# Kernel optimization log

Measured on AMD Instinct MI355X. Metric: run time of the kernel, lower is better.

## Reference

```python
import jax, jax.numpy as jnp
import numpy as np

B, S, D, MEM, STRIDE = 8, 8192, 128, 128, 64

def setup_inputs() -> dict:
    key = jax.random.key(0)
    ks = jax.random.split(key, 6)
    scale = 0.01  # matches nn.init.normal_(w, 0.0, 0.01)
    x = jax.random.normal(ks[0], (B, S, D), dtype=jnp.float32)
    Wq = scale * jax.random.normal(ks[1], (D, D), dtype=jnp.float32)
    Wk = scale * jax.random.normal(ks[2], (D, D), dtype=jnp.float32)
    Wv = scale * jax.random.normal(ks[3], (MEM, D), dtype=jnp.float32)
    Wg_w = jnp.zeros((1, D), dtype=jnp.float32)       # W_g weight init zeros
    Wg_b = jnp.full((1,), -2.0, dtype=jnp.float32)    # W_g bias init -2.0
    Wout = scale * jax.random.normal(ks[4], (D, MEM), dtype=jnp.float32)
    return {"x": x, "Wq": Wq, "Wk": Wk, "Wv": Wv, "Wg_w": Wg_w, "Wg_b": Wg_b, "Wout": Wout}

def reference(x, Wq, Wk, Wv, Wg_w, Wg_b, Wout):
    b, s, d = x.shape
    nC = s // STRIDE  # S assumed divisible by stride
    q = x @ Wq.T                                  # [B,S,D]
    k = x @ Wk.T                                  # [B,S,D]
    v = x @ Wv.T                                  # [B,S,MEM]
    g = jax.nn.sigmoid(x @ Wg_w.T + Wg_b)         # [B,S,1]
    # chunk: leading scan axis nC
    qc = q.reshape(b, nC, STRIDE, d).transpose(1, 0, 2, 3)
    kc = k.reshape(b, nC, STRIDE, d).transpose(1, 0, 2, 3)
    vc = v.reshape(b, nC, STRIDE, MEM).transpose(1, 0, 2, 3)
    gc = g.reshape(b, nC, STRIDE, 1).transpose(1, 0, 2, 3)

    def step(M, chunk):
        qch, kch, vch, gch = chunk
        reads = jnp.einsum('bsd,bdm->bsm', qch, M)              # read before write
        write = jnp.einsum('bsd,bsm->bdm', kch * gch, vch)      # gated outer-product
        avg_gate = gch.mean(axis=1, keepdims=True)              # [B,1,1]
        M_new = (1.0 - avg_gate) * M + write
        return M_new, reads

    M0 = jnp.zeros((b, d, MEM), dtype=x.dtype)
    _, reads = jax.lax.scan(step, M0, (qc, kc, vc, gc))         # [nC,B,STRIDE,MEM]
    out = reads.transpose(1, 0, 2, 3).reshape(b, s, MEM)
    return out @ Wout.T                                         # [B,S,D]
```

## Files before the change

### kernel.cpp

```cpp
#include <hip/hip_runtime.h>

#define Bn 8
#define Sn 8192
#define Dn 128
#define NCn 128

typedef _Float16 f16;
typedef f16 f16x2 __attribute__((ext_vector_type(2)));
typedef f16 f16x4 __attribute__((ext_vector_type(4)));
typedef float f32x4 __attribute__((ext_vector_type(4)));

static __device__ __forceinline__ f32x4 mfma16(f16x4 a, f16x4 b, f32x4 c) {
  return __builtin_amdgcn_mfma_f32_16x16x16f16(a, b, c, 0, 0, 0);
}

union UU { uint4 u; f16x2 h[4]; };


__global__ __launch_bounds__(64) void k_prep(
    const float* __restrict__ Wq, const float* __restrict__ Wk,
    const float* __restrict__ Wv, const float* __restrict__ Wout,
    f16* __restrict__ Amat, f16* __restrict__ r2) {
  const int blk = blockIdx.x;
  const int which = blk >> 6;
  const int t = blk & 63, ti = t >> 3, tj = t & 7;
  const int lane = threadIdx.x & 63, r16 = lane & 15, g4 = lane >> 4;
  f32x4 acc = {};
  if (which == 0) {
#pragma unroll
    for (int kk = 0; kk < 8; ++kk) {
      f16x4 af, bf;
#pragma unroll
      for (int j = 0; j < 4; ++j) {
        af[j] = (f16)Wq[(kk * 16 + g4 * 4 + j) * 128 + ti * 16 + r16];
        bf[j] = (f16)Wk[(kk * 16 + g4 * 4 + j) * 128 + tj * 16 + r16];
      }
      acc = mfma16(af, bf, acc);
    }
  } else {
#pragma unroll
    for (int kk = 0; kk < 8; ++kk) {
      f16x4 af, bf;
      float4 a4 = *(const float4*)(Wout + (ti * 16 + r16) * 128 + kk * 16 + g4 * 4);
      af[0] = (f16)a4.x; af[1] = (f16)a4.y; af[2] = (f16)a4.z; af[3] = (f16)a4.w;
#pragma unroll
      for (int j = 0; j < 4; ++j)
        bf[j] = (f16)Wv[(kk * 16 + g4 * 4 + j) * 128 + tj * 16 + r16];
      acc = mfma16(af, bf, acc);
    }
  }
  f16* dst = which ? r2 : Amat;
#pragma unroll
  for (int j = 0; j < 4; ++j)
    dst[(ti * 16 + g4 * 4 + j) * 128 + tj * 16 + r16] = (f16)acc[j];
}

__global__ __launch_bounds__(512, 8) void k_phase1(
    const float* __restrict__ x, const float* __restrict__ gw, const float* __restrict__ gb,
    const f16* __restrict__ Amat, const f16* __restrict__ r2,
    f16x4* __restrict__ wtg, float* __restrict__ gavg) {
  __shared__ __align__(16) f16 Xs[64][136];
  __shared__ __align__(16) f16x4 vP[2048];
  __shared__ float gs[64];
  const int h = blockIdx.x;
  const int grp = h & 127, m = h >> 7;
  const int b = grp >> 4, seg = grp & 15;
  const int c = seg * 8 + m;
  const int tid = threadIdx.x;
  {
    int s = tid >> 3, sub = tid & 7;
    const float* xrow = x + ((size_t)b * Sn + (size_t)c * 64 + s) * Dn;
    float gpart = 0.f;
#pragma unroll
    for (int i = 0; i < 4; ++i) {
      int col = sub * 4 + i * 32;
      float4 v = *(const float4*)(xrow + col);
      float4 g = *(const float4*)(gw + col);
      gpart += v.x * g.x + v.y * g.y + v.z * g.z + v.w * g.w;
      f16x4 hh = {(f16)v.x, (f16)v.y, (f16)v.z, (f16)v.w};
      *(f16x4*)&Xs[s][col] = hh;
    }
    gpart += __shfl_xor(gpart, 1);
    gpart += __shfl_xor(gpart, 2);
    gpart += __shfl_xor(gpart, 4);
    if (sub == 0) gs[s] = 1.f / (1.f + __expf(-(gpart + gb[0])));
  }
  __syncthreads();
  if (tid == 0) {
    float sum = 0.f;
#pragma unroll
    for (int i = 0; i < 64; ++i) sum += gs[i];
    gavg[b * NCn + c] = sum * (1.f / 64.f);
  }
  const int w = tid >> 6, lane = tid & 63, r16 = lane & 15, g4 = lane >> 4;

  f32x4 uacc[4] = {}, vacc[4] = {};
#pragma unroll
  for (int kk = 0; kk < 8; ++kk) {
    f16x4 bu = *(const f16x4*)&Amat[(w * 16 + r16) * 128 + kk * 16 + g4 * 4];
    f16x4 bv = *(const f16x4*)&r2[(w * 16 + r16) * 128 + kk * 16 + g4 * 4];
#pragma unroll
    for (int mr = 0; mr < 4; ++mr) {
      f16x4 af = *(f16x4*)&Xs[mr * 16 + r16][kk * 16 + g4 * 4];
      uacc[mr] = mfma16(af, bu, uacc[mr]);
      vacc[mr] = mfma16(af, bv, vacc[mr]);
    }
  }
  f16x4 ua[4];
#pragma unroll
  for (int mr = 0; mr < 4; ++mr) {
    float g0 = gs[mr * 16 + g4 * 4 + 0], g1 = gs[mr * 16 + g4 * 4 + 1];
    float g2 = gs[mr * 16 + g4 * 4 + 2], g3 = gs[mr * 16 + g4 * 4 + 3];
    f16x4 uh = {(f16)(uacc[mr][0] * g0), (f16)(uacc[mr][1] * g1),
                (f16)(uacc[mr][2] * g2), (f16)(uacc[mr][3] * g3)};
    ua[mr] = uh;
    f16x4 vh = {(f16)vacc[mr][0], (f16)vacc[mr][1], (f16)vacc[mr][2], (f16)vacc[mr][3]};
    vP[(mr * 8 + w) * 64 + lane] = vh;
  }
  __syncthreads();

  f32x4 z[8] = {};
#pragma unroll
  for (int ks = 0; ks < 4; ++ks)
#pragma unroll
    for (int ct = 0; ct < 8; ++ct)
      z[ct] = mfma16(ua[ks], vP[(ks * 8 + ct) * 64 + lane], z[ct]);

  f16x4* wdst = wtg + (size_t)(b * NCn + c) * 4096;
#pragma unroll
  for (int ct = 0; ct < 8; ++ct) {
    f16x4 zh = {(f16)z[ct][0], (f16)z[ct][1], (f16)z[ct][2], (f16)z[ct][3]};
    wdst[(w * 8 + ct) * 64 + lane] = zh;
  }
}

__global__ __launch_bounds__(256) void k_scan(
    const uint* __restrict__ wtg, const float* __restrict__ gavg, uint* __restrict__ pbuf) {
  const int blk = blockIdx.x;
  const int b = blk >> 5;
  const int e = (blk & 31) * 256 + threadIdx.x;
  const uint* wp = wtg + (size_t)b * (NCn * 8192) + e;
  uint* pp = pbuf + (size_t)b * (15 * 8192) + e;
  const float* ga = gavg + b * NCn;
  float M0 = 0.f, M1 = 0.f;
  uint ubuf[32];
  float abuf[32];
#pragma unroll
  for (int i = 0; i < 32; ++i) {
    ubuf[i] = wp[(size_t)i * 8192];
    abuf[i] = ga[i];
  }
  for (int g = 0; g < 4; ++g) {
    uint un[32];
    float an[32];
    if (g < 3) {
#pragma unroll
      for (int i = 0; i < 32; ++i) {
        un[i] = wp[(size_t)((g + 1) * 32 + i) * 8192];
        an[i] = ga[(g + 1) * 32 + i];
      }
    }
#pragma unroll
    for (int i = 0; i < 32; ++i) {
      int cc = g * 32 + i;
      f16x2 wv = __builtin_bit_cast(f16x2, ubuf[i]);
      float dd = 1.f - abuf[i];
      M0 = dd * M0 + (float)wv[0];
      M1 = dd * M1 + (float)wv[1];
      if ((cc & 7) == 7 && cc < 120) {
        f16x2 mv = {(f16)M0, (f16)M1};
        pp[(size_t)(cc >> 3) * 8192] = __builtin_bit_cast(uint, mv);
      }
    }
    if (g < 3) {
#pragma unroll
      for (int i = 0; i < 32; ++i) { ubuf[i] = un[i]; abuf[i] = an[i]; }
    }
  }
}

__global__ __launch_bounds__(512, 8) void k_out(
    const float* __restrict__ x, const uint4* __restrict__ wtg4,
    const uint4* __restrict__ pbuf4, const float* __restrict__ gavg,
    float* __restrict__ outp) {
  __shared__ __align__(16) f16 Xs[64][136];
  __shared__ __align__(16) f16x4 zP[2048];
  const int h = blockIdx.x;
  const int grp = h & 127, m = h >> 7;
  const int b = grp >> 4, seg = grp & 15;
  const int c = seg * 8 + m;
  const int tid = threadIdx.x;
  {
    int s = tid >> 3, sub = tid & 7;
    const float* xrow = x + ((size_t)b * Sn + (size_t)c * 64 + s) * Dn;
#pragma unroll
    for (int i = 0; i < 4; ++i) {
      int col = sub * 4 + i * 32;
      float4 v = *(const float4*)(xrow + col);
      f16x4 hh = {(f16)v.x, (f16)v.y, (f16)v.z, (f16)v.w};
      *(f16x4*)&Xs[s][col] = hh;
    }
  }
  float d[8], sfac[8];
#pragma unroll
  for (int t = 0; t < 8; ++t)
    d[t] = (t < m) ? (1.f - gavg[b * NCn + seg * 8 + t]) : 1.f;
  sfac[7] = 1.f;
#pragma unroll
  for (int t = 6; t >= 0; --t) sfac[t] = sfac[t + 1] * d[t + 1];
  const float sP = sfac[0] * d[0];

  const uint4* Zbase = wtg4 + (size_t)(b * NCn + seg * 8) * 2048;
  const uint4* Pp = pbuf4 + (size_t)(b * 15 + (seg > 0 ? seg - 1 : 0)) * 2048;

  const int w = tid >> 6, lane = tid & 63, r16 = lane & 15, g4 = lane >> 4;
  const int mr = w & 3, cb = (w >> 2) * 4;
  f32x4 acc[4] = {};

#pragma unroll
  for (int half = 0; half < 2; ++half) {
    if (half) __syncthreads();
#pragma unroll
    for (int i = 0; i < 2; ++i) {
      int idx = tid + i * 512;
      int src = half * 1024 + idx;
      float a8[8] = {0.f, 0.f, 0.f, 0.f, 0.f, 0.f, 0.f, 0.f};
      if (seg > 0) {
        UU z; z.u = Pp[src];
#pragma unroll
        for (int q = 0; q < 4; ++q) {
          a8[2 * q] += sP * (float)z.h[q][0];
          a8[2 * q + 1] += sP * (float)z.h[q][1];
        }
      }
#pragma unroll
      for (int t = 0; t < 8; ++t)
        if (t < m) {
          UU z; z.u = Zbase[(size_t)t * 2048 + src];
#pragma unroll
          for (int q = 0; q < 4; ++q) {
            a8[2 * q] += sfac[t] * (float)z.h[q][0];
            a8[2 * q + 1] += sfac[t] * (float)z.h[q][1];
          }
        }
      UU o;
#pragma unroll
      for (int q = 0; q < 4; ++q)
        o.h[q] = (f16x2){(f16)a8[2 * q], (f16)a8[2 * q + 1]};
      ((uint4*)zP)[idx] = o.u;
    }
    __syncthreads();
#pragma unroll
    for (int kk = 0; kk < 4; ++kk) {
      f16x4 af = *(f16x4*)&Xs[mr * 16 + r16][(half * 4 + kk) * 16 + g4 * 4];
#pragma unroll
      for (int t = 0; t < 4; ++t)
        acc[t] = mfma16(af, zP[(kk * 8 + cb + t) * 64 + lane], acc[t]);
    }
  }
  float* obase = outp + ((size_t)b * Sn + (size_t)c * 64 + mr * 16 + g4 * 4) * Dn;
#pragma unroll
  for (int t = 0; t < 4; ++t)
#pragma unroll
    for (int j = 0; j < 4; ++j)
      obase[(size_t)j * Dn + (cb + t) * 16 + r16] = acc[t][j];
}

extern "C" void kernel_launch(void* const* d_in, const int* in_sizes, int n_in,
                              void* d_out, int out_size, void* d_ws, size_t ws_size,
                              hipStream_t stream) {
  const float* x = (const float*)d_in[0];
  const float* Wq = (const float*)d_in[1];
  const float* Wk = (const float*)d_in[2];
  const float* Wv = (const float*)d_in[3];
  const float* gw = (const float*)d_in[4];
  const float* gb = (const float*)d_in[5];
  const float* Wout = (const float*)d_in[6];

  char* ws = (char*)d_ws;
  f16* Amat = (f16*)(ws + 0);
  f16* r2 = (f16*)(ws + 32768);
  float* gavg = (float*)(ws + 65536);
  f16* wtg = (f16*)(ws + 69632);
  f16* pbuf = (f16*)(ws + 69632 + 33554432);

  k_prep<<<dim3(128), dim3(64), 0, stream>>>(Wq, Wk, Wv, Wout, Amat, r2);
  k_phase1<<<dim3(Bn * NCn), dim3(512), 0, stream>>>(x, gw, gb, Amat, r2, (f16x4*)wtg, gavg);
  k_scan<<<dim3(256), dim3(256), 0, stream>>>((const uint*)wtg, gavg, (uint*)pbuf);
  k_out<<<dim3(Bn * NCn), dim3(512), 0, stream>>>(x, (const uint4*)wtg, (const uint4*)pbuf,
                                                  gavg, (float*)d_out);
}
```

Before: 64.29 us.

## Fuse all four stages into one cooperative kernel with grid syncs

```diff
diff --git a/kernel.cpp b/kernel.cpp
--- a/kernel.cpp
+++ b/kernel.cpp
@@ -1,4 +1,7 @@
 #include <hip/hip_runtime.h>
+#include <hip/hip_cooperative_groups.h>
+
+namespace cg = cooperative_groups;
 
 #define Bn 8
 #define Sn 8192
@@ -16,6 +19,251 @@
 
 union UU { uint4 u; f16x2 h[4]; };
 
+
+__global__ __launch_bounds__(512, 4) void k_fused(
+    const float* __restrict__ x, const float* __restrict__ gw, const float* __restrict__ gb,
+    const float* __restrict__ Wq, const float* __restrict__ Wk,
+    const float* __restrict__ Wv, const float* __restrict__ Wout,
+    f16* __restrict__ Amat, f16* __restrict__ r2, float* __restrict__ gavg,
+    f16x4* __restrict__ wtg, uint* __restrict__ pbuf, float* __restrict__ outp) {
+  cg::grid_group grid = cg::this_grid();
+  __shared__ __align__(16) char raw[34048];
+  f16(*Xs)[136] = (f16(*)[136])raw;
+  f16x4* vP = (f16x4*)(raw + 17408);
+  float* gs = (float*)(raw + 33792);
+
+  const int blk = blockIdx.x, tid = threadIdx.x;
+  const int w = tid >> 6, lane = tid & 63, r16 = lane & 15, g4 = lane >> 4;
+  const int grp = blk & 127, mbase = blk >> 7;
+  const int b = grp >> 4, seg = grp & 15;
+
+  if (blk < 64 && w < 2) {
+    const int ti = blk >> 3, tj = blk & 7;
+    f32x4 acc = {};
+    if (w == 0) {
+#pragma unroll
+      for (int kk = 0; kk < 8; ++kk) {
+        f16x4 af, bf;
+#pragma unroll
+        for (int j = 0; j < 4; ++j) {
+          af[j] = (f16)Wq[(kk * 16 + g4 * 4 + j) * 128 + ti * 16 + r16];
+          bf[j] = (f16)Wk[(kk * 16 + g4 * 4 + j) * 128 + tj * 16 + r16];
+        }
+        acc = mfma16(af, bf, acc);
+      }
+#pragma unroll
+      for (int j = 0; j < 4; ++j)
+        Amat[(ti * 16 + g4 * 4 + j) * 128 + tj * 16 + r16] = (f16)acc[j];
+    } else {
+#pragma unroll
+      for (int kk = 0; kk < 8; ++kk) {
+        f16x4 af, bf;
+        float4 a4 = *(const float4*)(Wout + (ti * 16 + r16) * 128 + kk * 16 + g4 * 4);
+        af[0] = (f16)a4.x; af[1] = (f16)a4.y; af[2] = (f16)a4.z; af[3] = (f16)a4.w;
+#pragma unroll
+        for (int j = 0; j < 4; ++j)
+          bf[j] = (f16)Wv[(kk * 16 + g4 * 4 + j) * 128 + tj * 16 + r16];
+        acc = mfma16(af, bf, acc);
+      }
+#pragma unroll
+      for (int j = 0; j < 4; ++j)
+        r2[(ti * 16 + g4 * 4 + j) * 128 + tj * 16 + r16] = (f16)acc[j];
+    }
+  }
+  grid.sync();
+
+#pragma unroll
+  for (int mm = 0; mm < 2; ++mm) {
+    const int c = seg * 8 + mbase + mm * 4;
+    {
+      int s = tid >> 3, sub = tid & 7;
+      const float* xrow = x + ((size_t)b * Sn + (size_t)c * 64 + s) * Dn;
+      float gpart = 0.f;
+#pragma unroll
+      for (int i = 0; i < 4; ++i) {
+        int col = sub * 4 + i * 32;
+        float4 v = *(const float4*)(xrow + col);
+        float4 g = *(const float4*)(gw + col);
+        gpart += v.x * g.x + v.y * g.y + v.z * g.z + v.w * g.w;
+        f16x4 hh = {(f16)v.x, (f16)v.y, (f16)v.z, (f16)v.w};
+        *(f16x4*)&Xs[s][col] = hh;
+      }
+      gpart += __shfl_xor(gpart, 1);
+      gpart += __shfl_xor(gpart, 2);
+      gpart += __shfl_xor(gpart, 4);
+      if (sub == 0) gs[s] = 1.f / (1.f + __expf(-(gpart + gb[0])));
+    }
+    __syncthreads();
+    if (tid == 0) {
+      float sum = 0.f;
+#pragma unroll
+      for (int i = 0; i < 64; ++i) sum += gs[i];
+      gavg[b * NCn + c] = sum * (1.f / 64.f);
+    }
+    f32x4 uacc[4] = {}, vacc[4] = {};
+#pragma unroll
+    for (int kk = 0; kk < 8; ++kk) {
+      f16x4 bu = *(const f16x4*)&Amat[(w * 16 + r16) * 128 + kk * 16 + g4 * 4];
+      f16x4 bv = *(const f16x4*)&r2[(w * 16 + r16) * 128 + kk * 16 + g4 * 4];
+#pragma unroll
+      for (int mr = 0; mr < 4; ++mr) {
+        f16x4 af = *(f16x4*)&Xs[mr * 16 + r16][kk * 16 + g4 * 4];
+        uacc[mr] = mfma16(af, bu, uacc[mr]);
+        vacc[mr] = mfma16(af, bv, vacc[mr]);
+      }
+    }
+    f16x4 ua[4];
+#pragma unroll
+    for (int mr = 0; mr < 4; ++mr) {
+      float g0 = gs[mr * 16 + g4 * 4 + 0], g1 = gs[mr * 16 + g4 * 4 + 1];
+      float g2 = gs[mr * 16 + g4 * 4 + 2], g3 = gs[mr * 16 + g4 * 4 + 3];
+      f16x4 uh = {(f16)(uacc[mr][0] * g0), (f16)(uacc[mr][1] * g1),
+                  (f16)(uacc[mr][2] * g2), (f16)(uacc[mr][3] * g3)};
+      ua[mr] = uh;
+      f16x4 vh = {(f16)vacc[mr][0], (f16)vacc[mr][1], (f16)vacc[mr][2], (f16)vacc[mr][3]};
+      vP[(mr * 8 + w) * 64 + lane] = vh;
+    }
+    __syncthreads();
+    f32x4 z[8] = {};
+#pragma unroll
+    for (int ks = 0; ks < 4; ++ks)
+#pragma unroll
+      for (int ct = 0; ct < 8; ++ct)
+        z[ct] = mfma16(ua[ks], vP[(ks * 8 + ct) * 64 + lane], z[ct]);
+    f16x4* wdst = wtg + (size_t)(b * NCn + c) * 4096;
+#pragma unroll
+    for (int ct = 0; ct < 8; ++ct) {
+      f16x4 zh = {(f16)z[ct][0], (f16)z[ct][1], (f16)z[ct][2], (f16)z[ct][3]};
+      wdst[(w * 8 + ct) * 64 + lane] = zh;
+    }
+    __syncthreads();
+  }
+  grid.sync();
+
+  if (blk < 128) {
+    const int sid = blk * 512 + tid;
+    const int sb = sid >> 13, e = sid & 8191;
+    const uint* wp = (const uint*)wtg + (size_t)sb * (NCn * 8192) + e;
+    uint* pp = pbuf + (size_t)sb * (15 * 8192) + e;
+    const float* ga = gavg + sb * NCn;
+    float M0 = 0.f, M1 = 0.f;
+    uint ubuf[16];
+    float abuf[16];
+#pragma unroll
+    for (int i = 0; i < 16; ++i) {
+      ubuf[i] = wp[(size_t)i * 8192];
+      abuf[i] = ga[i];
+    }
+    for (int g = 0; g < 8; ++g) {
+      uint un[16];
+      float an[16];
+      if (g < 7) {
+#pragma unroll
+        for (int i = 0; i < 16; ++i) {
+          un[i] = wp[(size_t)((g + 1) * 16 + i) * 8192];
+          an[i] = ga[(g + 1) * 16 + i];
+        }
+      }
+#pragma unroll
+      for (int i = 0; i < 16; ++i) {
+        int cc = g * 16 + i;
+        f16x2 wv = __builtin_bit_cast(f16x2, ubuf[i]);
+        float dd = 1.f - abuf[i];
+        M0 = dd * M0 + (float)wv[0];
+        M1 = dd * M1 + (float)wv[1];
+        if ((cc & 7) == 7 && cc < 120) {
+          f16x2 mv = {(f16)M0, (f16)M1};
+          pp[(size_t)(cc >> 3) * 8192] = __builtin_bit_cast(uint, mv);
+        }
+      }
+      if (g < 7) {
+#pragma unroll
+        for (int i = 0; i < 16; ++i) { ubuf[i] = un[i]; abuf[i] = an[i]; }
+      }
+    }
+  }
+  grid.sync();
+
+  const uint4* wtg4 = (const uint4*)wtg;
+  const uint4* pbuf4 = (const uint4*)pbuf;
+  f16x4* zP = vP;
+#pragma unroll
+  for (int mm = 0; mm < 2; ++mm) {
+    const int m = mbase + mm * 4;
+    const int c = seg * 8 + m;
+    if (mm) __syncthreads();
+    {
+      int s = tid >> 3, sub = tid & 7;
+      const float* xrow = x + ((size_t)b * Sn + (size_t)c * 64 + s) * Dn;
+#pragma unroll
+      for (int i = 0; i < 4; ++i) {
+        int col = sub * 4 + i * 32;
+        float4 v = *(const float4*)(xrow + col);
+        f16x4 hh = {(f16)v.x, (f16)v.y, (f16)v.z, (f16)v.w};
+        *(f16x4*)&Xs[s][col] = hh;
+      }
+    }
+    float d[8], sfac[8];
+#pragma unroll
+    for (int t = 0; t < 8; ++t)
+      d[t] = (t < m) ? (1.f - gavg[b * NCn + seg * 8 + t]) : 1.f;
+    sfac[7] = 1.f;
+#pragma unroll
+    for (int t = 6; t >= 0; --t) sfac[t] = sfac[t + 1] * d[t + 1];
+    const float sP = sfac[0] * d[0];
+    const uint4* Zbase = wtg4 + (size_t)(b * NCn + seg * 8) * 2048;
+    const uint4* Pp = pbuf4 + (size_t)(b * 15 + (seg > 0 ? seg - 1 : 0)) * 2048;
+    const int mr = w & 3, cb = (w >> 2) * 4;
+    f32x4 acc[4] = {};
+#pragma unroll
+    for (int half = 0; half < 2; ++half) {
+      if (half) __syncthreads();
+#pragma unroll
+      for (int i = 0; i < 2; ++i) {
+        int idx = tid + i * 512;
+        int src = half * 1024 + idx;
+        float a8[8] = {0.f, 0.f, 0.f, 0.f, 0.f, 0.f, 0.f, 0.f};
+        if (seg > 0) {
+          UU z; z.u = Pp[src];
+#pragma unroll
+          for (int q = 0; q < 4; ++q) {
+            a8[2 * q] += sP * (float)z.h[q][0];
+            a8[2 * q + 1] += sP * (float)z.h[q][1];
+          }
+        }
+#pragma unroll
+        for (int t = 0; t < 8; ++t)
+          if (t < m) {
+            UU z; z.u = Zbase[(size_t)t * 2048 + src];
+#pragma unroll
+            for (int q = 0; q < 4; ++q) {
+              a8[2 * q] += sfac[t] * (float)z.h[q][0];
+              a8[2 * q + 1] += sfac[t] * (float)z.h[q][1];
+            }
+          }
+        UU o;
+#pragma unroll
+        for (int q = 0; q < 4; ++q)
+          o.h[q] = (f16x2){(f16)a8[2 * q], (f16)a8[2 * q + 1]};
+        ((uint4*)zP)[idx] = o.u;
+      }
+      __syncthreads();
+#pragma unroll
+      for (int kk = 0; kk < 4; ++kk) {
+        f16x4 af = *(f16x4*)&Xs[mr * 16 + r16][(half * 4 + kk) * 16 + g4 * 4];
+#pragma unroll
+        for (int t = 0; t < 4; ++t)
+          acc[t] = mfma16(af, zP[(kk * 8 + cb + t) * 64 + lane], acc[t]);
+      }
+    }
+    float* obase = outp + ((size_t)b * Sn + (size_t)c * 64 + mr * 16 + g4 * 4) * Dn;
+#pragma unroll
+    for (int t = 0; t < 4; ++t)
+#pragma unroll
+      for (int j = 0; j < 4; ++j)
+        obase[(size_t)j * Dn + (cb + t) * 16 + r16] = acc[t][j];
+  }
+}
 
 __global__ __launch_bounds__(64) void k_prep(
     const float* __restrict__ Wq, const float* __restrict__ Wk,
@@ -93,7 +341,6 @@
     gavg[b * NCn + c] = sum * (1.f / 64.f);
   }
   const int w = tid >> 6, lane = tid & 63, r16 = lane & 15, g4 = lane >> 4;
-
   f32x4 uacc[4] = {}, vacc[4] = {};
 #pragma unroll
   for (int kk = 0; kk < 8; ++kk) {
@@ -118,14 +365,12 @@
     vP[(mr * 8 + w) * 64 + lane] = vh;
   }
   __syncthreads();
-
   f32x4 z[8] = {};
 #pragma unroll
   for (int ks = 0; ks < 4; ++ks)
 #pragma unroll
     for (int ct = 0; ct < 8; ++ct)
       z[ct] = mfma16(ua[ks], vP[(ks * 8 + ct) * 64 + lane], z[ct]);
-
   f16x4* wdst = wtg + (size_t)(b * NCn + c) * 4096;
 #pragma unroll
   for (int ct = 0; ct < 8; ++ct) {
@@ -209,14 +454,11 @@
 #pragma unroll
   for (int t = 6; t >= 0; --t) sfac[t] = sfac[t + 1] * d[t + 1];
   const float sP = sfac[0] * d[0];
-
   const uint4* Zbase = wtg4 + (size_t)(b * NCn + seg * 8) * 2048;
   const uint4* Pp = pbuf4 + (size_t)(b * 15 + (seg > 0 ? seg - 1 : 0)) * 2048;
-
   const int w = tid >> 6, lane = tid & 63, r16 = lane & 15, g4 = lane >> 4;
   const int mr = w & 3, cb = (w >> 2) * 4;
   f32x4 acc[4] = {};
-
 #pragma unroll
   for (int half = 0; half < 2; ++half) {
     if (half) __syncthreads();
@@ -283,10 +525,20 @@
   float* gavg = (float*)(ws + 65536);
   f16* wtg = (f16*)(ws + 69632);
   f16* pbuf = (f16*)(ws + 69632 + 33554432);
-
-  k_prep<<<dim3(128), dim3(64), 0, stream>>>(Wq, Wk, Wv, Wout, Amat, r2);
-  k_phase1<<<dim3(Bn * NCn), dim3(512), 0, stream>>>(x, gw, gb, Amat, r2, (f16x4*)wtg, gavg);
-  k_scan<<<dim3(256), dim3(256), 0, stream>>>((const uint*)wtg, gavg, (uint*)pbuf);
-  k_out<<<dim3(Bn * NCn), dim3(512), 0, stream>>>(x, (const uint4*)wtg, (const uint4*)pbuf,
-                                                  gavg, (float*)d_out);
-}
+  float* outp = (float*)d_out;
+
+  f16x4* wtg4 = (f16x4*)wtg;
+  uint* pbufu = (uint*)pbuf;
+  void* args[] = {(void*)&x, (void*)&gw, (void*)&gb, (void*)&Wq, (void*)&Wk,
+                  (void*)&Wv, (void*)&Wout, (void*)&Amat, (void*)&r2,
+                  (void*)&gavg, (void*)&wtg4, (void*)&pbufu, (void*)&outp};
+  hipError_t err = hipLaunchCooperativeKernel((const void*)k_fused, dim3(512), dim3(512),
+                                              args, 0, stream);
+  if (err != hipSuccess) {
+    k_prep<<<dim3(128), dim3(64), 0, stream>>>(Wq, Wk, Wv, Wout, Amat, r2);
+    k_phase1<<<dim3(Bn * NCn), dim3(512), 0, stream>>>(x, gw, gb, Amat, r2, (f16x4*)wtg, gavg);
+    k_scan<<<dim3(256), dim3(256), 0, stream>>>((const uint*)wtg, gavg, (uint*)pbuf);
+    k_out<<<dim3(Bn * NCn), dim3(512), 0, stream>>>(x, (const uint4*)wtg, (const uint4*)pbuf,
+                                                    gavg, (float*)d_out);
+  }
+}
```

Result: slower. 226.6 us (+252.5%).

## Replace per-chunk state reconstruction with sequential in-segment state update in output kernel

Applied to the files above, without the earlier changes.

```diff
diff --git a/kernel.cpp b/kernel.cpp
--- a/kernel.cpp
+++ b/kernel.cpp
@@ -14,7 +14,7 @@
   return __builtin_amdgcn_mfma_f32_16x16x16f16(a, b, c, 0, 0, 0);
 }
 
-union UU { uint4 u; f16x2 h[4]; };
+union UU { uint4 u; f16x2 h[4]; f16x4 q[2]; };
 
 
 __global__ __launch_bounds__(64) void k_prep(
@@ -58,7 +58,7 @@
 __global__ __launch_bounds__(512, 8) void k_phase1(
     const float* __restrict__ x, const float* __restrict__ gw, const float* __restrict__ gb,
     const f16* __restrict__ Amat, const f16* __restrict__ r2,
-    f16x4* __restrict__ wtg, float* __restrict__ gavg) {
+    f16x4* __restrict__ wtg, float* __restrict__ gavg, f16* __restrict__ xh) {
   __shared__ __align__(16) f16 Xs[64][136];
   __shared__ __align__(16) f16x4 vP[2048];
   __shared__ float gs[64];
@@ -70,6 +70,7 @@
   {
     int s = tid >> 3, sub = tid & 7;
     const float* xrow = x + ((size_t)b * Sn + (size_t)c * 64 + s) * Dn;
+    f16* xhrow = xh + (size_t)(b * NCn + c) * 8192 + s * 128;
     float gpart = 0.f;
 #pragma unroll
     for (int i = 0; i < 4; ++i) {
@@ -79,6 +80,7 @@
       gpart += v.x * g.x + v.y * g.y + v.z * g.z + v.w * g.w;
       f16x4 hh = {(f16)v.x, (f16)v.y, (f16)v.z, (f16)v.w};
       *(f16x4*)&Xs[s][col] = hh;
+      *(f16x4*)&xhrow[col] = hh;
     }
     gpart += __shfl_xor(gpart, 1);
     gpart += __shfl_xor(gpart, 2);
@@ -93,7 +95,6 @@
     gavg[b * NCn + c] = sum * (1.f / 64.f);
   }
   const int w = tid >> 6, lane = tid & 63, r16 = lane & 15, g4 = lane >> 4;
-
   f32x4 uacc[4] = {}, vacc[4] = {};
 #pragma unroll
   for (int kk = 0; kk < 8; ++kk) {
@@ -118,14 +119,12 @@
     vP[(mr * 8 + w) * 64 + lane] = vh;
   }
   __syncthreads();
-
   f32x4 z[8] = {};
 #pragma unroll
   for (int ks = 0; ks < 4; ++ks)
 #pragma unroll
     for (int ct = 0; ct < 8; ++ct)
       z[ct] = mfma16(ua[ks], vP[(ks * 8 + ct) * 64 + lane], z[ct]);
-
   f16x4* wdst = wtg + (size_t)(b * NCn + c) * 4096;
 #pragma unroll
   for (int ct = 0; ct < 8; ++ct) {
@@ -179,91 +178,93 @@
   }
 }
 
-__global__ __launch_bounds__(512, 8) void k_out(
-    const float* __restrict__ x, const uint4* __restrict__ wtg4,
+__global__ __launch_bounds__(512, 4) void k_outseg(
+    const f16* __restrict__ xh, const uint4* __restrict__ wtg4,
     const uint4* __restrict__ pbuf4, const float* __restrict__ gavg,
     float* __restrict__ outp) {
   __shared__ __align__(16) f16 Xs[64][136];
-  __shared__ __align__(16) f16x4 zP[2048];
-  const int h = blockIdx.x;
-  const int grp = h & 127, m = h >> 7;
-  const int b = grp >> 4, seg = grp & 15;
-  const int c = seg * 8 + m;
+  __shared__ __align__(16) float Mf[4096];
+  __shared__ __align__(16) f16x4 Mh4[1024];
+  const int blk = blockIdx.x;
+  const int q = blk & 3, seg = (blk >> 2) & 15, b = blk >> 6;
   const int tid = threadIdx.x;
-  {
-    int s = tid >> 3, sub = tid & 7;
-    const float* xrow = x + ((size_t)b * Sn + (size_t)c * 64 + s) * Dn;
-#pragma unroll
-    for (int i = 0; i < 4; ++i) {
-      int col = sub * 4 + i * 32;
-      float4 v = *(const float4*)(xrow + col);
-      f16x4 hh = {(f16)v.x, (f16)v.y, (f16)v.z, (f16)v.w};
-      *(f16x4*)&Xs[s][col] = hh;
-    }
-  }
-  float d[8], sfac[8];
-#pragma unroll
-  for (int t = 0; t < 8; ++t)
-    d[t] = (t < m) ? (1.f - gavg[b * NCn + seg * 8 + t]) : 1.f;
-  sfac[7] = 1.f;
-#pragma unroll
-  for (int t = 6; t >= 0; --t) sfac[t] = sfac[t + 1] * d[t + 1];
-  const float sP = sfac[0] * d[0];
-
-  const uint4* Zbase = wtg4 + (size_t)(b * NCn + seg * 8) * 2048;
-  const uint4* Pp = pbuf4 + (size_t)(b * 15 + (seg > 0 ? seg - 1 : 0)) * 2048;
-
   const int w = tid >> 6, lane = tid & 63, r16 = lane & 15, g4 = lane >> 4;
-  const int mr = w & 3, cb = (w >> 2) * 4;
-  f32x4 acc[4] = {};
-
-#pragma unroll
-  for (int half = 0; half < 2; ++half) {
-    if (half) __syncthreads();
-#pragma unroll
-    for (int i = 0; i < 2; ++i) {
-      int idx = tid + i * 512;
-      int src = half * 1024 + idx;
-      float a8[8] = {0.f, 0.f, 0.f, 0.f, 0.f, 0.f, 0.f, 0.f};
-      if (seg > 0) {
-        UU z; z.u = Pp[src];
-#pragma unroll
-        for (int q = 0; q < 4; ++q) {
-          a8[2 * q] += sP * (float)z.h[q][0];
-          a8[2 * q + 1] += sP * (float)z.h[q][1];
-        }
-      }
-#pragma unroll
-      for (int t = 0; t < 8; ++t)
-        if (t < m) {
-          UU z; z.u = Zbase[(size_t)t * 2048 + src];
-#pragma unroll
-          for (int q = 0; q < 4; ++q) {
-            a8[2 * q] += sfac[t] * (float)z.h[q][0];
-            a8[2 * q + 1] += sfac[t] * (float)z.h[q][1];
-          }
-        }
-      UU o;
-#pragma unroll
-      for (int q = 0; q < 4; ++q)
-        o.h[q] = (f16x2){(f16)a8[2 * q], (f16)a8[2 * q + 1]};
-      ((uint4*)zP)[idx] = o.u;
+  const int mr = w & 3, tq = w >> 2;
+
+  const int lt = tid >> 5;
+  const int gtile = (lt >> 1) * 8 + q * 2 + (lt & 1);
+  const int slot = tid & 31;
+
+  float dseg[8];
+#pragma unroll
+  for (int t = 0; t < 8; ++t) dseg[t] = 1.f - gavg[b * NCn + seg * 8 + t];
+
+  float4* Mf4 = (float4*)Mf;
+  if (seg > 0) {
+    UU z; z.u = pbuf4[(size_t)(b * 15 + seg - 1) * 2048 + gtile * 32 + slot];
+#pragma unroll
+    for (int h2 = 0; h2 < 2; ++h2) {
+      float4 mv = {(float)z.h[2 * h2][0], (float)z.h[2 * h2][1],
+                   (float)z.h[2 * h2 + 1][0], (float)z.h[2 * h2 + 1][1]};
+      Mf4[tid * 2 + h2] = mv;
+    }
+  } else {
+    float4 zz = {0.f, 0.f, 0.f, 0.f};
+    Mf4[tid * 2] = zz;
+    Mf4[tid * 2 + 1] = zz;
+  }
+
+  const uint4* Zseg = wtg4 + (size_t)(b * NCn + seg * 8) * 2048;
+  const f16* xhseg = xh + (size_t)(b * NCn + seg * 8) * 8192;
+
+  for (int m = 0; m < 8; ++m) {
+    {
+      const uint4* xs4 = (const uint4*)(xhseg + (size_t)m * 8192);
+      int row = tid >> 3, col = (tid & 7) * 16;
+      uint4 a = xs4[tid * 2];
+      uint4 bq = xs4[tid * 2 + 1];
+      *(uint4*)&Xs[row][col] = a;
+      *(uint4*)&Xs[row][col + 8] = bq;
+    }
+#pragma unroll
+    for (int h2 = 0; h2 < 2; ++h2) {
+      float4 mv = Mf4[tid * 2 + h2];
+      f16x4 hh = {(f16)mv.x, (f16)mv.y, (f16)mv.z, (f16)mv.w};
+      Mh4[tid * 2 + h2] = hh;
     }
     __syncthreads();
-#pragma unroll
-    for (int kk = 0; kk < 4; ++kk) {
-      f16x4 af = *(f16x4*)&Xs[mr * 16 + r16][(half * 4 + kk) * 16 + g4 * 4];
-#pragma unroll
-      for (int t = 0; t < 4; ++t)
-        acc[t] = mfma16(af, zP[(kk * 8 + cb + t) * 64 + lane], acc[t]);
-    }
-  }
-  float* obase = outp + ((size_t)b * Sn + (size_t)c * 64 + mr * 16 + g4 * 4) * Dn;
-#pragma unroll
-  for (int t = 0; t < 4; ++t)
-#pragma unroll
-    for (int j = 0; j < 4; ++j)
-      obase[(size_t)j * Dn + (cb + t) * 16 + r16] = acc[t][j];
+
+    f32x4 acc = {};
+#pragma unroll
+    for (int kk = 0; kk < 8; ++kk) {
+      f16x4 af = *(f16x4*)&Xs[mr * 16 + r16][kk * 16 + g4 * 4];
+      f16x4 bf = Mh4[(kk * 2 + tq) * 64 + lane];
+      acc = mfma16(af, bf, acc);
+    }
+
+    {
+      UU z; z.u = Zseg[(size_t)m * 2048 + gtile * 32 + slot];
+      float dd = dseg[m];
+#pragma unroll
+      for (int h2 = 0; h2 < 2; ++h2) {
+        float4 mv = Mf4[tid * 2 + h2];
+        mv.x = dd * mv.x + (float)z.h[2 * h2][0];
+        mv.y = dd * mv.y + (float)z.h[2 * h2][1];
+        mv.z = dd * mv.z + (float)z.h[2 * h2 + 1][0];
+        mv.w = dd * mv.w + (float)z.h[2 * h2 + 1][1];
+        Mf4[tid * 2 + h2] = mv;
+      }
+    }
+
+    {
+      const int c = seg * 8 + m;
+      float* ob = outp + ((size_t)b * Sn + (size_t)c * 64 + mr * 16 + g4 * 4) * Dn +
+                  (q * 2 + tq) * 16 + r16;
+#pragma unroll
+      for (int j = 0; j < 4; ++j) ob[(size_t)j * Dn] = acc[j];
+    }
+    __syncthreads();
+  }
 }
 
 extern "C" void kernel_launch(void* const* d_in, const int* in_sizes, int n_in,
@@ -282,11 +283,13 @@
   f16* r2 = (f16*)(ws + 32768);
   float* gavg = (float*)(ws + 65536);
   f16* wtg = (f16*)(ws + 69632);
-  f16* pbuf = (f16*)(ws + 69632 + 33554432);
+  f16* pbuf = (f16*)(ws + 33624064);
+  f16* xh = (f16*)(ws + 37556224);
 
   k_prep<<<dim3(128), dim3(64), 0, stream>>>(Wq, Wk, Wv, Wout, Amat, r2);
-  k_phase1<<<dim3(Bn * NCn), dim3(512), 0, stream>>>(x, gw, gb, Amat, r2, (f16x4*)wtg, gavg);
+  k_phase1<<<dim3(Bn * NCn), dim3(512), 0, stream>>>(x, gw, gb, Amat, r2, (f16x4*)wtg,
+                                                     gavg, xh);
   k_scan<<<dim3(256), dim3(256), 0, stream>>>((const uint*)wtg, gavg, (uint*)pbuf);
-  k_out<<<dim3(Bn * NCn), dim3(512), 0, stream>>>(x, (const uint4*)wtg, (const uint4*)pbuf,
-                                                  gavg, (float*)d_out);
-}
+  k_outseg<<<dim3(512), dim3(512), 0, stream>>>(xh, (const uint4*)wtg, (const uint4*)pbuf,
+                                                gavg, (float*)d_out);
+}
```

Result: no change. 64.92 us (+1.0%).
